# Kernel optimization log

Hardware: AMD Instinct MI355X
Metric: run time of the kernel (lower is better)

Reference implementation:

```python
import jax, jax.numpy as jnp
import numpy as np


def setup_inputs() -> dict:
    key = jax.random.key(0)
    k0, k1, k2, k3 = jax.random.split(key, 4)
    B, T, Din, H, Dout = 8, 4096, 1024, 1024, 1024
    x = jax.random.normal(k0, (B, T, Din), dtype=jnp.float32)
    # Linear weights stored torch-style as [out_features, in_features]
    W_hg = jax.random.normal(k1, (2 * H, Din), dtype=jnp.float32) * 0.02
    W_out = jax.random.normal(k2, (Dout, H), dtype=jnp.float32) * 0.02
    # episode-reset flags, 0/1 floats, shape [B,T,1] (expanded over channels)
    is_init = jax.random.bernoulli(k3, 0.01, (B, T, 1)).astype(jnp.float32)
    h_0 = jnp.zeros((B, 1, H), dtype=jnp.float32)
    return {"x": x, "W_hg": W_hg, "W_out": W_out, "is_init": is_init, "h_0": h_0}


def _mingru_scan(gate, hidden, is_init, h_0):
    # Linear recurrence h_t = (1-g_t) h_{t-1} + g_t * hidden_t, with resets.
    A = 1.0 - gate               # [B,T,H]
    Bv = gate * hidden           # [B,T,H]
    r = jnp.broadcast_to(is_init, Bv.shape)

    def combine(c1, c2):
        a1, b1, r1 = c1
        a2, b2, r2 = c2
        reset = r2 > 0
        a = jnp.where(reset, a2, a2 * a1)
        b = jnp.where(reset, b2, a2 * b1 + b2)
        return a, b, jnp.minimum(r1 + r2, 1.0)  # clamp(max=1)

    # Prepending the identity element then dropping it (as the torch code does)
    # is a no-op for an inclusive associative scan, so scan T elements directly.
    A_out, B_out, _ = jax.lax.associative_scan(combine, (A, Bv, r), axis=1)
    return A_out * h_0 + B_out   # h_0 is [B,1,H], broadcasts over T


def reference(x, W_hg, W_out, is_init, h_0):
    hg = jnp.einsum("btd,hd->bth", x, W_hg)          # [B,T,2H]
    hidden, gate = jnp.split(hg, 2, axis=-1)
    gate = jax.nn.sigmoid(gate)
    h = _mingru_scan(gate, hidden, is_init, h_0)      # [B,T,H]
    h_n = h[:, -1:]                                   # [B,1,H]
    out = jnp.einsum("bth,oh->bto", h, W_out)         # [B,T,Dout]
    return out, h_n
```

## Files before the change

kernel.cpp:

```cpp
#include <hip/hip_runtime.h>
#include <stdint.h>

#define B_DIM 8
#define T_DIM 4096
#define K_DIM 1024
#define H_DIM 1024
#define M_DIM (B_DIM * T_DIM)
#define CHUNK 64
#define NCHUNK (T_DIM / CHUNK)

typedef __attribute__((ext_vector_type(8))) short s16x8;
typedef __attribute__((ext_vector_type(4))) float f32x4;

__device__ __forceinline__ unsigned short f2b(float f) {
    union { float f; uint32_t u; } c; c.f = f;
    uint32_t r = (c.u + 0x7fffu + ((c.u >> 16) & 1u)) >> 16;
    return (unsigned short)r;
}
__device__ __forceinline__ float b2f(unsigned short u) {
    union { uint32_t u; float f; } c; c.u = ((uint32_t)u) << 16;
    return c.f;
}

__device__ __forceinline__ void gload_lds16(const unsigned short* g,
                                            unsigned short* l) {
    __builtin_amdgcn_global_load_lds(
        (__attribute__((address_space(1))) void*)g,
        (__attribute__((address_space(3))) void*)l, 16, 0, 0);
}

__device__ __forceinline__ void bar() {
    asm volatile("s_barrier" ::: "memory");
}


__global__ void cvt_f32_bf16(const float* __restrict__ src,
                             unsigned short* __restrict__ dst, int n4) {
    int stride = gridDim.x * blockDim.x;
    for (int i = blockIdx.x * blockDim.x + threadIdx.x; i < n4; i += stride) {
        float4 v = ((const float4*)src)[i];
        ushort4 o;
        o.x = f2b(v.x); o.y = f2b(v.y); o.z = f2b(v.z); o.w = f2b(v.w);
        ((ushort4*)dst)[i] = o;
    }
}

__global__ void prep_whg(const float* __restrict__ W,
                         unsigned short* __restrict__ Wp) {
    int i = blockIdx.x * blockDim.x + threadIdx.x;
    int total = 2 * H_DIM * K_DIM / 4;
    if (i >= total) return;
    int e = i * 4;
    int n = e >> 10;
    int k = e & 1023;
    int src = (n & 1) ? (H_DIM + (n >> 1)) : (n >> 1);
    float4 v = *(const float4*)&W[(size_t)src * K_DIM + k];
    ushort4 o;
    o.x = f2b(v.x); o.y = f2b(v.y); o.z = f2b(v.z); o.w = f2b(v.w);
    *(ushort4*)&Wp[(size_t)n * K_DIM + k] = o;
}


template <int EPI>
__global__ __launch_bounds__(512, 2) void gemm256(
    const unsigned short* __restrict__ A,
    const unsigned short* __restrict__ Bm,
    float* __restrict__ C,
    unsigned short* __restrict__ Sa,
    unsigned short* __restrict__ Sb,
    int N) {
    __shared__ unsigned short As[2][256 * 64];
    __shared__ unsigned short Bs[2][256 * 64];
    const int K = K_DIM;
    const int KT = K / 64;

    const int gx = gridDim.x;
    const int nwg = gx * gridDim.y;
    const int orig = blockIdx.y * gx + blockIdx.x;
    const int cpx = nwg >> 3;
    const int wg = (orig & 7) * cpx + (orig >> 3);
    const int m0 = (wg / gx) * 256;
    const int n0 = (wg % gx) * 256;

    const int t = threadIdx.x;
    const int lane = t & 63;
    const int w = t >> 6;
    const int wm = w >> 2, wn = w & 3;

    const int lrow = lane >> 3;
    const int lslot = (lane & 7) ^ lrow;

    const int l15 = lane & 15;
    const int rq = lane >> 4;
    const int rx = l15 & 7;

    f32x4 acc[8][4];
#pragma unroll
    for (int m = 0; m < 8; m++)
#pragma unroll
        for (int n = 0; n < 4; n++) acc[m][n] = (f32x4){0.f, 0.f, 0.f, 0.f};

    auto stageA = [&](int kt, int buf, int j) {
        const int seg = j * 8 + w;
        const int row = seg * 8 + lrow;
        gload_lds16(&A[(size_t)(m0 + row) * K + kt * 64 + lslot * 8],
                    &As[buf][seg * 512]);
    };
    auto stageB = [&](int kt, int buf, int j) {
        const int seg = j * 8 + w;
        const int row = seg * 8 + lrow;
        gload_lds16(&Bm[(size_t)(n0 + row) * K + kt * 64 + lslot * 8],
                    &Bs[buf][seg * 512]);
    };

    s16x8 af[4], bf[4];

#define LDA(buf, mi, ks) \
    (*(const s16x8*)&As[buf][(wm * 128 + (mi) * 16 + l15) * 64 + (((rq + (ks) * 4) ^ rx) * 8)])
#define LDB(buf, ni, ks) \
    (*(const s16x8*)&Bs[buf][(wn * 64 + (ni) * 16 + l15) * 64 + (((rq + (ks) * 4) ^ rx) * 8)])

#define MFMA16(MB)                                                          \
    __builtin_amdgcn_s_setprio(1);                                          \
    _Pragma("unroll") for (int m = 0; m < 4; m++)                           \
        _Pragma("unroll") for (int n = 0; n < 4; n++)                       \
            acc[MB + m][n] = __builtin_amdgcn_mfma_f32_16x16x32_bf16(       \
                af[m], bf[n], acc[MB + m][n], 0, 0, 0);                     \
    __builtin_amdgcn_s_setprio(0);

    {
#pragma unroll
        for (int j = 0; j < 4; j++) stageA(0, 0, j);
#pragma unroll
        for (int j = 0; j < 4; j++) stageB(0, 0, j);
        asm volatile("s_waitcnt vmcnt(0)" ::: "memory");
        bar();
    }

    for (int kt = 0; kt < KT; ++kt) {
        const int buf = kt & 1;
        const int nb = buf ^ 1;
        const bool nx = (kt + 1 < KT);
#pragma unroll
        for (int m = 0; m < 4; m++) af[m] = LDA(buf, m, 0);
#pragma unroll
        for (int n = 0; n < 4; n++) bf[n] = LDB(buf, n, 0);
        if (nx) { stageA(kt + 1, nb, 0); stageA(kt + 1, nb, 1); stageB(kt + 1, nb, 0); }
        bar();
        MFMA16(0);
        bar();
#pragma unroll
        for (int m = 0; m < 4; m++) af[m] = LDA(buf, m + 4, 0);
        if (nx) { stageA(kt + 1, nb, 2); stageA(kt + 1, nb, 3); stageB(kt + 1, nb, 1); }
        bar();
        MFMA16(4);
        bar();
#pragma unroll
        for (int m = 0; m < 4; m++) af[m] = LDA(buf, m, 1);
#pragma unroll
        for (int n = 0; n < 4; n++) bf[n] = LDB(buf, n, 1);
        if (nx) { stageB(kt + 1, nb, 2); stageB(kt + 1, nb, 3); }
        bar();
        MFMA16(0);
        bar();
#pragma unroll
        for (int m = 0; m < 4; m++) af[m] = LDA(buf, m + 4, 1);
        asm volatile("s_waitcnt vmcnt(0)" ::: "memory");
        bar();
        MFMA16(4);
        bar();
    }

    const int lr4 = rq * 4;
#pragma unroll
    for (int m = 0; m < 8; m++) {
#pragma unroll
        for (int n = 0; n < 4; n++) {
#pragma unroll
            for (int r = 0; r < 4; r++) {
                const int row = m0 + wm * 128 + m * 16 + lr4 + r;
                const int col = n0 + wn * 64 + n * 16 + l15;
                float v = acc[m][n][r];
                if (EPI == 0) {
                    C[(size_t)row * N + col] = v;
                } else {
                    float o = __shfl_xor(v, 1);
                    int ch = col >> 1;
                    if ((lane & 1) == 0) {
                        float g = 1.f / (1.f + __expf(-o));
                        Sb[(size_t)row * H_DIM + ch] = f2b(g * v);
                    } else {
                        float g = 1.f / (1.f + __expf(-v));
                        Sa[(size_t)row * H_DIM + ch] = f2b(1.f - g);
                    }
                }
            }
        }
    }
#undef LDA
#undef LDB
#undef MFMA16
}


__global__ __launch_bounds__(256) void scan_chunks(
    const unsigned short* __restrict__ Sa, const unsigned short* __restrict__ Sb,
    const float* __restrict__ is_init,
    float* __restrict__ CA, float* __restrict__ CB, float* __restrict__ CR) {
    int idx = blockIdx.x * 256 + threadIdx.x;
    int ch = idx & (H_DIM - 1);
    int chunk = (idx >> 10) & (NCHUNK - 1);
    int b = idx >> 16;
    int t0 = chunk * CHUNK;
    size_t base = ((size_t)b * T_DIM + t0) * H_DIM + ch;
    const float* ii = is_init + (size_t)b * T_DIM + t0;
    float A = 1.f, Bv = 0.f;
    int rf = 0;
    for (int i = 0; i < CHUNK; i++) {
        float a = b2f(Sa[base + (size_t)i * H_DIM]);
        float bb = b2f(Sb[base + (size_t)i * H_DIM]);
        bool rst = ii[i] > 0.f;
        A = rst ? a : a * A;
        Bv = rst ? bb : fmaf(a, Bv, bb);
        rf |= (int)rst;
    }
    size_t o = ((size_t)b * NCHUNK + chunk) * H_DIM + ch;
    CA[o] = A;
    CB[o] = Bv;
    if (ch == 0) CR[b * NCHUNK + chunk] = (float)rf;
}

__global__ void scan_tops(const float* __restrict__ CA, const float* __restrict__ CB,
                          const float* __restrict__ CR,
                          float* __restrict__ PA, float* __restrict__ PB) {
    int idx = blockIdx.x * blockDim.x + threadIdx.x;
    if (idx >= B_DIM * H_DIM) return;
    int ch = idx & (H_DIM - 1);
    int b = idx >> 10;
    float A = 1.f, Bv = 0.f;
    for (int c = 0; c < NCHUNK; c++) {
        size_t o = ((size_t)b * NCHUNK + c) * H_DIM + ch;
        PA[o] = A;
        PB[o] = Bv;
        float a = CA[o], bb = CB[o];
        bool rst = CR[b * NCHUNK + c] > 0.f;
        float nA = rst ? a : a * A;
        float nB = rst ? bb : fmaf(a, Bv, bb);
        A = nA; Bv = nB;
    }
}

__global__ __launch_bounds__(256) void scan_apply(
    const unsigned short* __restrict__ Sa, const unsigned short* __restrict__ Sb,
    const float* __restrict__ is_init,
    const float* __restrict__ PA, const float* __restrict__ PB,
    const float* __restrict__ h0,
    unsigned short* __restrict__ hb, float* __restrict__ hn) {
    int idx = blockIdx.x * 256 + threadIdx.x;
    int ch = idx & (H_DIM - 1);
    int chunk = (idx >> 10) & (NCHUNK - 1);
    int b = idx >> 16;
    int t0 = chunk * CHUNK;
    size_t base = ((size_t)b * T_DIM + t0) * H_DIM + ch;
    const float* ii = is_init + (size_t)b * T_DIM + t0;
    size_t po = ((size_t)b * NCHUNK + chunk) * H_DIM + ch;
    float A = PA[po], Bv = PB[po];
    float h0v = h0[b * H_DIM + ch];
    float h = 0.f;
    for (int i = 0; i < CHUNK; i++) {
        float a = b2f(Sa[base + (size_t)i * H_DIM]);
        float bb = b2f(Sb[base + (size_t)i * H_DIM]);
        bool rst = ii[i] > 0.f;
        A = rst ? a : a * A;
        Bv = rst ? bb : fmaf(a, Bv, bb);
        h = fmaf(A, h0v, Bv);
        hb[base + (size_t)i * H_DIM] = f2b(h);
    }
    if (chunk == NCHUNK - 1) hn[b * H_DIM + ch] = h;
}


extern "C" void kernel_launch(void* const* d_in, const int* in_sizes, int n_in,
                              void* d_out, int out_size, void* d_ws, size_t ws_size,
                              hipStream_t stream) {
    const float* x       = (const float*)d_in[0];
    const float* W_hg    = (const float*)d_in[1];
    const float* W_out   = (const float*)d_in[2];
    const float* is_init = (const float*)d_in[3];
    const float* h0      = (const float*)d_in[4];
    float* out = (float*)d_out;
    float* hn  = out + (size_t)M_DIM * H_DIM;

    char* ws = (char*)d_ws;
    size_t off = 0;
    auto alloc = [&](size_t bytes) {
        void* p = ws + off;
        off += (bytes + 255) & ~(size_t)255;
        return p;
    };
    unsigned short* xb  = (unsigned short*)alloc((size_t)M_DIM * K_DIM * 2);
    unsigned short* Wp  = (unsigned short*)alloc((size_t)2 * H_DIM * K_DIM * 2);
    unsigned short* Wob = (unsigned short*)alloc((size_t)H_DIM * K_DIM * 2);
    unsigned short* Sa  = (unsigned short*)alloc((size_t)M_DIM * H_DIM * 2);
    unsigned short* Sb  = (unsigned short*)alloc((size_t)M_DIM * H_DIM * 2);
    float* CA = (float*)alloc((size_t)B_DIM * NCHUNK * H_DIM * 4);
    float* CB = (float*)alloc((size_t)B_DIM * NCHUNK * H_DIM * 4);
    float* CR = (float*)alloc((size_t)B_DIM * NCHUNK * 4);
    float* PA = (float*)alloc((size_t)B_DIM * NCHUNK * H_DIM * 4);
    float* PB = (float*)alloc((size_t)B_DIM * NCHUNK * H_DIM * 4);
    unsigned short* hb = xb;

    cvt_f32_bf16<<<2048, 256, 0, stream>>>(x, xb, M_DIM * K_DIM / 4);
    prep_whg<<<(2 * H_DIM * K_DIM / 4 + 255) / 256, 256, 0, stream>>>(W_hg, Wp);
    cvt_f32_bf16<<<1024, 256, 0, stream>>>(W_out, Wob, H_DIM * K_DIM / 4);

    gemm256<1><<<dim3(2048 / 256, M_DIM / 256), 512, 0, stream>>>(
        xb, Wp, nullptr, Sa, Sb, 2048);

    scan_chunks<<<(B_DIM * NCHUNK * H_DIM) / 256, 256, 0, stream>>>(
        Sa, Sb, is_init, CA, CB, CR);
    scan_tops<<<(B_DIM * H_DIM + 255) / 256, 256, 0, stream>>>(CA, CB, CR, PA, PB);
    scan_apply<<<(B_DIM * NCHUNK * H_DIM) / 256, 256, 0, stream>>>(
        Sa, Sb, is_init, PA, PB, h0, hb, hn);

    gemm256<0><<<dim3(1024 / 256, M_DIM / 256), 512, 0, stream>>>(
        hb, Wob, out, nullptr, nullptr, 1024);
}
```

Measured before the change: 374.6 us.

## Restructure GEMM inner loop into two phases with both k-slices loaded

The k-tile loop in the bf16 MFMA GEMM now has two phases instead of four. Each phase loads both k-substeps of A and B fragments from LDS into separate register sets, then issues 32 MFMAs per barrier pair. Global-to-LDS staging is regrouped so all of A is prefetched in the first phase and all of B in the second, with explicit lgkmcnt waits and sched_barriers. The aim is fewer workgroup barriers and longer MFMA runs, at the cost of extra VGPRs for the doubled fragment registers, which could lower occupancy.

```diff
diff --git a/kernel.cpp b/kernel.cpp
--- a/kernel.cpp
+++ b/kernel.cpp
@@ -113,19 +113,23 @@
                     &Bs[buf][seg * 512]);
     };
 
-    s16x8 af[4], bf[4];
+    s16x8 af0[4], af1[4], bf0[4], bf1[4];
 
 #define LDA(buf, mi, ks) \
     (*(const s16x8*)&As[buf][(wm * 128 + (mi) * 16 + l15) * 64 + (((rq + (ks) * 4) ^ rx) * 8)])
 #define LDB(buf, ni, ks) \
     (*(const s16x8*)&Bs[buf][(wn * 64 + (ni) * 16 + l15) * 64 + (((rq + (ks) * 4) ^ rx) * 8)])
 
-#define MFMA16(MB)                                                          \
+#define MFMA32(MB)                                                          \
     __builtin_amdgcn_s_setprio(1);                                          \
     _Pragma("unroll") for (int m = 0; m < 4; m++)                           \
         _Pragma("unroll") for (int n = 0; n < 4; n++)                       \
             acc[MB + m][n] = __builtin_amdgcn_mfma_f32_16x16x32_bf16(       \
-                af[m], bf[n], acc[MB + m][n], 0, 0, 0);                     \
+                af0[m], bf0[n], acc[MB + m][n], 0, 0, 0);                   \
+    _Pragma("unroll") for (int m = 0; m < 4; m++)                           \
+        _Pragma("unroll") for (int n = 0; n < 4; n++)                       \
+            acc[MB + m][n] = __builtin_amdgcn_mfma_f32_16x16x32_bf16(       \
+                af1[m], bf1[n], acc[MB + m][n], 0, 0, 0);                   \
     __builtin_amdgcn_s_setprio(0);
 
     {
@@ -142,32 +146,31 @@
         const int nb = buf ^ 1;
         const bool nx = (kt + 1 < KT);
 #pragma unroll
-        for (int m = 0; m < 4; m++) af[m] = LDA(buf, m, 0);
-#pragma unroll
-        for (int n = 0; n < 4; n++) bf[n] = LDB(buf, n, 0);
-        if (nx) { stageA(kt + 1, nb, 0); stageA(kt + 1, nb, 1); stageB(kt + 1, nb, 0); }
-        bar();
-        MFMA16(0);
-        bar();
-#pragma unroll
-        for (int m = 0; m < 4; m++) af[m] = LDA(buf, m + 4, 0);
-        if (nx) { stageA(kt + 1, nb, 2); stageA(kt + 1, nb, 3); stageB(kt + 1, nb, 1); }
-        bar();
-        MFMA16(4);
-        bar();
-#pragma unroll
-        for (int m = 0; m < 4; m++) af[m] = LDA(buf, m, 1);
-#pragma unroll
-        for (int n = 0; n < 4; n++) bf[n] = LDB(buf, n, 1);
-        if (nx) { stageB(kt + 1, nb, 2); stageB(kt + 1, nb, 3); }
-        bar();
-        MFMA16(0);
-        bar();
-#pragma unroll
-        for (int m = 0; m < 4; m++) af[m] = LDA(buf, m + 4, 1);
+        for (int m = 0; m < 4; m++) { af0[m] = LDA(buf, m, 0); af1[m] = LDA(buf, m, 1); }
+#pragma unroll
+        for (int n = 0; n < 4; n++) { bf0[n] = LDB(buf, n, 0); bf1[n] = LDB(buf, n, 1); }
+        if (nx) {
+#pragma unroll
+            for (int j = 0; j < 4; j++) stageA(kt + 1, nb, j);
+        }
+        asm volatile("s_waitcnt lgkmcnt(8)" ::: "memory");
+        bar();
+        asm volatile("s_waitcnt lgkmcnt(0)" ::: "memory");
+        __builtin_amdgcn_sched_barrier(0);
+        MFMA32(0);
+        bar();
+#pragma unroll
+        for (int m = 0; m < 4; m++) { af0[m] = LDA(buf, m + 4, 0); af1[m] = LDA(buf, m + 4, 1); }
+        if (nx) {
+#pragma unroll
+            for (int j = 0; j < 4; j++) stageB(kt + 1, nb, j);
+        }
+        asm volatile("s_waitcnt lgkmcnt(4)" ::: "memory");
+        bar();
+        asm volatile("s_waitcnt lgkmcnt(0)" ::: "memory");
+        __builtin_amdgcn_sched_barrier(0);
+        MFMA32(4);
         asm volatile("s_waitcnt vmcnt(0)" ::: "memory");
-        bar();
-        MFMA16(4);
         bar();
     }
 
@@ -199,7 +202,7 @@
     }
 #undef LDA
 #undef LDB
-#undef MFMA16
+#undef MFMA32
 }
 
 
```

After: 396.2 us. 1.06x slower.

## Restage GEMM LDS into four half-K slots with deeper vmcnt-gated prefetch

Applied to the files above, without the earlier changes.

Splits each 64-wide K tile into two 32-wide halves held in a 4-slot LDS ring, using a lane-contiguous layout per 16-row block instead of the XOR-swizzled 64-wide layout. Global-to-LDS loads are issued further ahead and throttled with partial vmcnt waits rather than a full drain each iteration. Explicit lgkmcnt waits and sched barriers fence each MFMA phase. The aim is to hide more global-load latency. The risks are LDS bank conflicts from dropping the swizzle and extra synchronisation overhead.

```diff
diff --git a/kernel.cpp b/kernel.cpp
--- a/kernel.cpp
+++ b/kernel.cpp
@@ -69,8 +69,8 @@
     unsigned short* __restrict__ Sa,
     unsigned short* __restrict__ Sb,
     int N) {
-    __shared__ unsigned short As[2][256 * 64];
-    __shared__ unsigned short Bs[2][256 * 64];
+    __shared__ unsigned short As4[4][256 * 32];
+    __shared__ unsigned short Bs4[4][256 * 32];
     const int K = K_DIM;
     const int KT = K / 64;
 
@@ -87,12 +87,11 @@
     const int w = t >> 6;
     const int wm = w >> 2, wn = w & 3;
 
-    const int lrow = lane >> 3;
-    const int lslot = (lane & 7) ^ lrow;
+    const int srow = lane & 15;
+    const int sq   = lane >> 4;
 
     const int l15 = lane & 15;
     const int rq = lane >> 4;
-    const int rx = l15 & 7;
 
     f32x4 acc[8][4];
 #pragma unroll
@@ -100,76 +99,75 @@
 #pragma unroll
         for (int n = 0; n < 4; n++) acc[m][n] = (f32x4){0.f, 0.f, 0.f, 0.f};
 
-    auto stageA = [&](int kt, int buf, int j) {
-        const int seg = j * 8 + w;
-        const int row = seg * 8 + lrow;
-        gload_lds16(&A[(size_t)(m0 + row) * K + kt * 64 + lslot * 8],
-                    &As[buf][seg * 512]);
+    auto stageA = [&](int kt, int ks, int j) {
+        const int slot = (2 * kt + ks) & 3;
+        const int row = j * 128 + w * 16 + srow;
+        const int gk  = kt * 64 + ks * 32 + sq * 8;
+        gload_lds16(&A[(size_t)(m0 + row) * K + gk],
+                    &As4[slot][(j * 128 + w * 16) * 32]);
     };
-    auto stageB = [&](int kt, int buf, int j) {
-        const int seg = j * 8 + w;
-        const int row = seg * 8 + lrow;
-        gload_lds16(&Bm[(size_t)(n0 + row) * K + kt * 64 + lslot * 8],
-                    &Bs[buf][seg * 512]);
+    auto stageB = [&](int kt, int ks, int j) {
+        const int slot = (2 * kt + ks) & 3;
+        const int row = j * 128 + w * 16 + srow;
+        const int gk  = kt * 64 + ks * 32 + sq * 8;
+        gload_lds16(&Bm[(size_t)(n0 + row) * K + gk],
+                    &Bs4[slot][(j * 128 + w * 16) * 32]);
     };
 
     s16x8 af[4], bf[4];
 
-#define LDA(buf, mi, ks) \
-    (*(const s16x8*)&As[buf][(wm * 128 + (mi) * 16 + l15) * 64 + (((rq + (ks) * 4) ^ rx) * 8)])
-#define LDB(buf, ni, ks) \
-    (*(const s16x8*)&Bs[buf][(wn * 64 + (ni) * 16 + l15) * 64 + (((rq + (ks) * 4) ^ rx) * 8)])
-
-#define MFMA16(MB)                                                          \
+#define LDAX(S, MI) \
+    (*(const s16x8*)&As4[S][(wm * 8 + (MI)) * 512 + rq * 128 + l15 * 8])
+#define LDBX(S, NI) \
+    (*(const s16x8*)&Bs4[S][(wn * 4 + (NI)) * 512 + rq * 128 + l15 * 8])
+
+#define LGKM0 do { asm volatile("s_waitcnt lgkmcnt(0)" ::: "memory"); \
+                   __builtin_amdgcn_sched_barrier(0); } while (0)
+#define VMW8 asm volatile("s_waitcnt vmcnt(8)" ::: "memory")
+#define VMW4 asm volatile("s_waitcnt vmcnt(4)" ::: "memory")
+#define VMW0 asm volatile("s_waitcnt vmcnt(0)" ::: "memory")
+
+#define PH_MFMA(MB) do {                                                    \
     __builtin_amdgcn_s_setprio(1);                                          \
-    _Pragma("unroll") for (int m = 0; m < 4; m++)                           \
-        _Pragma("unroll") for (int n = 0; n < 4; n++)                       \
-            acc[MB + m][n] = __builtin_amdgcn_mfma_f32_16x16x32_bf16(       \
-                af[m], bf[n], acc[MB + m][n], 0, 0, 0);                     \
-    __builtin_amdgcn_s_setprio(0);
-
-    {
-#pragma unroll
-        for (int j = 0; j < 4; j++) stageA(0, 0, j);
-#pragma unroll
-        for (int j = 0; j < 4; j++) stageB(0, 0, j);
-        asm volatile("s_waitcnt vmcnt(0)" ::: "memory");
-        bar();
-    }
-
-    for (int kt = 0; kt < KT; ++kt) {
-        const int buf = kt & 1;
-        const int nb = buf ^ 1;
-        const bool nx = (kt + 1 < KT);
-#pragma unroll
-        for (int m = 0; m < 4; m++) af[m] = LDA(buf, m, 0);
-#pragma unroll
-        for (int n = 0; n < 4; n++) bf[n] = LDB(buf, n, 0);
-        if (nx) { stageA(kt + 1, nb, 0); stageA(kt + 1, nb, 1); stageB(kt + 1, nb, 0); }
-        bar();
-        MFMA16(0);
-        bar();
-#pragma unroll
-        for (int m = 0; m < 4; m++) af[m] = LDA(buf, m + 4, 0);
-        if (nx) { stageA(kt + 1, nb, 2); stageA(kt + 1, nb, 3); stageB(kt + 1, nb, 1); }
-        bar();
-        MFMA16(4);
-        bar();
-#pragma unroll
-        for (int m = 0; m < 4; m++) af[m] = LDA(buf, m, 1);
-#pragma unroll
-        for (int n = 0; n < 4; n++) bf[n] = LDB(buf, n, 1);
-        if (nx) { stageB(kt + 1, nb, 2); stageB(kt + 1, nb, 3); }
-        bar();
-        MFMA16(0);
-        bar();
-#pragma unroll
-        for (int m = 0; m < 4; m++) af[m] = LDA(buf, m + 4, 1);
-        asm volatile("s_waitcnt vmcnt(0)" ::: "memory");
-        bar();
-        MFMA16(4);
-        bar();
-    }
+    _Pragma("unroll") for (int m_ = 0; m_ < 4; m_++)                        \
+        _Pragma("unroll") for (int n_ = 0; n_ < 4; n_++)                    \
+            acc[(MB) + m_][n_] = __builtin_amdgcn_mfma_f32_16x16x32_bf16(   \
+                af[m_], bf[n_], acc[(MB) + m_][n_], 0, 0, 0);               \
+    __builtin_amdgcn_s_setprio(0);                                          \
+} while (0)
+
+#define ISSUE_U(KT_, KS_) do {                                              \
+    stageA((KT_), (KS_), 0); stageA((KT_), (KS_), 1);                       \
+    stageB((KT_), (KS_), 0); stageB((KT_), (KS_), 1);                       \
+} while (0)
+
+#define TILE(KT_, ISS1, ISS3, VM2, VM4) do {                                \
+    const int s0_ = (2 * (KT_)) & 3, s1_ = (2 * (KT_) + 1) & 3;             \
+    _Pragma("unroll") for (int m_ = 0; m_ < 4; m_++) af[m_] = LDAX(s0_, m_);\
+    _Pragma("unroll") for (int n_ = 0; n_ < 4; n_++) bf[n_] = LDBX(s0_, n_);\
+    ISS1;                                                                   \
+    bar(); LGKM0; PH_MFMA(0); bar();                                        \
+    _Pragma("unroll") for (int m_ = 0; m_ < 4; m_++) af[m_] = LDAX(s0_, m_ + 4); \
+    bar(); LGKM0; PH_MFMA(4); VM2; bar();                                   \
+    _Pragma("unroll") for (int m_ = 0; m_ < 4; m_++) af[m_] = LDAX(s1_, m_);\
+    _Pragma("unroll") for (int n_ = 0; n_ < 4; n_++) bf[n_] = LDBX(s1_, n_);\
+    ISS3;                                                                   \
+    bar(); LGKM0; PH_MFMA(0); bar();                                        \
+    _Pragma("unroll") for (int m_ = 0; m_ < 4; m_++) af[m_] = LDAX(s1_, m_ + 4); \
+    bar(); LGKM0; PH_MFMA(4); VM4; bar();                                   \
+} while (0)
+
+    ISSUE_U(0, 0);
+    ISSUE_U(0, 1);
+    ISSUE_U(1, 0);
+    VMW8;
+    bar();
+
+    for (int kt = 0; kt < KT - 2; ++kt) {
+        TILE(kt, ISSUE_U(kt + 1, 1), ISSUE_U(kt + 2, 0), VMW8, VMW8);
+    }
+    TILE(KT - 2, ISSUE_U(KT - 1, 1), ((void)0), VMW8, VMW4);
+    TILE(KT - 1, ((void)0), ((void)0), VMW0, ((void)0));
 
     const int lr4 = rq * 4;
 #pragma unroll
@@ -197,9 +195,11 @@
             }
         }
     }
-#undef LDA
-#undef LDB
-#undef MFMA16
+#undef LDAX
+#undef LDBX
+#undef TILE
+#undef PH_MFMA
+#undef ISSUE_U
 }
 
 
```

New measurement: 474.6 us. +26.7%, slower.

## Fuse three-pass chunked scan into single-pass decoupled look-back kernel

Applied to the files above, without the earlier changes.

Replaces the chunk-reduce, top-level scan and apply kernels with one kernel that claims chunks through an atomic ticket. Each chunk keeps its 64 gate/value pairs in registers, publishes its aggregate or inclusive end state, and walks back over predecessor status flags. The GEMM epilogue now writes a packed bf16 (a,b) pair per element, so the scan reads a single 32-bit word instead of two separate arrays. The aim is to read Sa/Sb once instead of twice and to drop the serial per-batch tops kernel and two launches. In exchange it adds spin-waiting on flags, a 64-register array per thread, and a dependence on forward-progress ordering via the ticket counter.

```diff
diff --git a/kernel.cpp b/kernel.cpp
--- a/kernel.cpp
+++ b/kernel.cpp
@@ -60,14 +60,18 @@
     *(ushort4*)&Wp[(size_t)n * K_DIM + k] = o;
 }
 
+__global__ void zero_flags(int* f, int n) {
+    int i = blockIdx.x * blockDim.x + threadIdx.x;
+    if (i < n) f[i] = 0;
+}
+
 
 template <int EPI>
 __global__ __launch_bounds__(512, 2) void gemm256(
     const unsigned short* __restrict__ A,
     const unsigned short* __restrict__ Bm,
     float* __restrict__ C,
-    unsigned short* __restrict__ Sa,
-    unsigned short* __restrict__ Sb,
+    uint32_t* __restrict__ Sab,
     int N) {
     __shared__ unsigned short As[2][256 * 64];
     __shared__ unsigned short Bs[2][256 * 64];
@@ -185,13 +189,11 @@
                     C[(size_t)row * N + col] = v;
                 } else {
                     float o = __shfl_xor(v, 1);
-                    int ch = col >> 1;
                     if ((lane & 1) == 0) {
                         float g = 1.f / (1.f + __expf(-o));
-                        Sb[(size_t)row * H_DIM + ch] = f2b(g * v);
-                    } else {
-                        float g = 1.f / (1.f + __expf(-v));
-                        Sa[(size_t)row * H_DIM + ch] = f2b(1.f - g);
+                        uint32_t pk = (uint32_t)f2b(1.f - g) |
+                                      ((uint32_t)f2b(g * v) << 16);
+                        Sab[(size_t)row * H_DIM + (col >> 1)] = pk;
                     }
                 }
             }
@@ -203,80 +205,111 @@
 }
 
 
-__global__ __launch_bounds__(256) void scan_chunks(
-    const unsigned short* __restrict__ Sa, const unsigned short* __restrict__ Sb,
-    const float* __restrict__ is_init,
-    float* __restrict__ CA, float* __restrict__ CB, float* __restrict__ CR) {
-    int idx = blockIdx.x * 256 + threadIdx.x;
-    int ch = idx & (H_DIM - 1);
-    int chunk = (idx >> 10) & (NCHUNK - 1);
-    int b = idx >> 16;
-    int t0 = chunk * CHUNK;
-    size_t base = ((size_t)b * T_DIM + t0) * H_DIM + ch;
+__global__ __launch_bounds__(1024) void scan_fused(
+    const uint32_t* __restrict__ Sab, const float* __restrict__ is_init,
+    const float* __restrict__ h0,
+    uint32_t* __restrict__ aggA, uint32_t* __restrict__ aggB,
+    uint32_t* __restrict__ hend, int* __restrict__ status,
+    int* __restrict__ ticket,
+    unsigned short* __restrict__ hb, float* __restrict__ hn) {
+    __shared__ int s_tick;
+    __shared__ int s_st;
+    if (threadIdx.x == 0) s_tick = atomicAdd(ticket, 1);
+    __syncthreads();
+    const int bc = s_tick;
+    const int b = bc >> 6;
+    const int c = bc & 63;
+    const int ch = threadIdx.x;
+    const int t0 = c * CHUNK;
+    const size_t base = ((size_t)b * T_DIM + t0) * H_DIM + ch;
     const float* ii = is_init + (size_t)b * T_DIM + t0;
+    const float h0v = h0[b * H_DIM + ch];
+
+    uint32_t d[CHUNK];
+#pragma unroll
+    for (int i = 0; i < CHUNK; i++) d[i] = Sab[base + (size_t)i * H_DIM];
+
     float A = 1.f, Bv = 0.f;
     int rf = 0;
+#pragma unroll
     for (int i = 0; i < CHUNK; i++) {
-        float a = b2f(Sa[base + (size_t)i * H_DIM]);
-        float bb = b2f(Sb[base + (size_t)i * H_DIM]);
+        float a = b2f((unsigned short)(d[i] & 0xffffu));
+        float bb = b2f((unsigned short)(d[i] >> 16));
         bool rst = ii[i] > 0.f;
         A = rst ? a : a * A;
         Bv = rst ? bb : fmaf(a, Bv, bb);
         rf |= (int)rst;
     }
-    size_t o = ((size_t)b * NCHUNK + chunk) * H_DIM + ch;
-    CA[o] = A;
-    CB[o] = Bv;
-    if (ch == 0) CR[b * NCHUNK + chunk] = (float)rf;
-}
-
-__global__ void scan_tops(const float* __restrict__ CA, const float* __restrict__ CB,
-                          const float* __restrict__ CR,
-                          float* __restrict__ PA, float* __restrict__ PB) {
-    int idx = blockIdx.x * blockDim.x + threadIdx.x;
-    if (idx >= B_DIM * H_DIM) return;
-    int ch = idx & (H_DIM - 1);
-    int b = idx >> 10;
-    float A = 1.f, Bv = 0.f;
-    for (int c = 0; c < NCHUNK; c++) {
-        size_t o = ((size_t)b * NCHUNK + c) * H_DIM + ch;
-        PA[o] = A;
-        PB[o] = Bv;
-        float a = CA[o], bb = CB[o];
-        bool rst = CR[b * NCHUNK + c] > 0.f;
-        float nA = rst ? a : a * A;
-        float nB = rst ? bb : fmaf(a, Bv, bb);
-        A = nA; Bv = nB;
-    }
-}
-
-__global__ __launch_bounds__(256) void scan_apply(
-    const unsigned short* __restrict__ Sa, const unsigned short* __restrict__ Sb,
-    const float* __restrict__ is_init,
-    const float* __restrict__ PA, const float* __restrict__ PB,
-    const float* __restrict__ h0,
-    unsigned short* __restrict__ hb, float* __restrict__ hn) {
-    int idx = blockIdx.x * 256 + threadIdx.x;
-    int ch = idx & (H_DIM - 1);
-    int chunk = (idx >> 10) & (NCHUNK - 1);
-    int b = idx >> 16;
-    int t0 = chunk * CHUNK;
-    size_t base = ((size_t)b * T_DIM + t0) * H_DIM + ch;
-    const float* ii = is_init + (size_t)b * T_DIM + t0;
-    size_t po = ((size_t)b * NCHUNK + chunk) * H_DIM + ch;
-    float A = PA[po], Bv = PB[po];
-    float h0v = h0[b * H_DIM + ch];
-    float h = 0.f;
+
+    const bool inc_now = (c == 0) || rf;
+    if (inc_now) {
+        __hip_atomic_store(&hend[(size_t)bc * H_DIM + ch],
+                           __float_as_uint(fmaf(A, h0v, Bv)),
+                           __ATOMIC_RELAXED, __HIP_MEMORY_SCOPE_AGENT);
+    } else {
+        __hip_atomic_store(&aggA[(size_t)bc * H_DIM + ch], __float_as_uint(A),
+                           __ATOMIC_RELAXED, __HIP_MEMORY_SCOPE_AGENT);
+        __hip_atomic_store(&aggB[(size_t)bc * H_DIM + ch], __float_as_uint(Bv),
+                           __ATOMIC_RELAXED, __HIP_MEMORY_SCOPE_AGENT);
+    }
+    __syncthreads();
+    if (threadIdx.x == 0)
+        __hip_atomic_store(&status[bc], inc_now ? 2 : 1,
+                           __ATOMIC_RELEASE, __HIP_MEMORY_SCOPE_AGENT);
+
+    float hentry = h0v;
+    if (c > 0) {
+        float sA = 1.f, sB = 0.f;
+        int p = bc - 1;
+        for (;;) {
+            if (threadIdx.x == 0) {
+                int st;
+                while ((st = __hip_atomic_load(&status[p], __ATOMIC_ACQUIRE,
+                                               __HIP_MEMORY_SCOPE_AGENT)) == 0)
+                    __builtin_amdgcn_s_sleep(4);
+                s_st = st;
+            }
+            __syncthreads();
+            int st = s_st;
+            __syncthreads();
+            if (st == 2) {
+                float he = __uint_as_float(__hip_atomic_load(
+                    &hend[(size_t)p * H_DIM + ch], __ATOMIC_RELAXED,
+                    __HIP_MEMORY_SCOPE_AGENT));
+                hentry = fmaf(sA, he, sB);
+                break;
+            }
+            float ea = __uint_as_float(__hip_atomic_load(
+                &aggA[(size_t)p * H_DIM + ch], __ATOMIC_RELAXED,
+                __HIP_MEMORY_SCOPE_AGENT));
+            float eb = __uint_as_float(__hip_atomic_load(
+                &aggB[(size_t)p * H_DIM + ch], __ATOMIC_RELAXED,
+                __HIP_MEMORY_SCOPE_AGENT));
+            sB = fmaf(sA, eb, sB);
+            sA = sA * ea;
+            p--;
+        }
+    }
+
+    float h = hentry;
+#pragma unroll
     for (int i = 0; i < CHUNK; i++) {
-        float a = b2f(Sa[base + (size_t)i * H_DIM]);
-        float bb = b2f(Sb[base + (size_t)i * H_DIM]);
+        float a = b2f((unsigned short)(d[i] & 0xffffu));
+        float bb = b2f((unsigned short)(d[i] >> 16));
         bool rst = ii[i] > 0.f;
-        A = rst ? a : a * A;
-        Bv = rst ? bb : fmaf(a, Bv, bb);
-        h = fmaf(A, h0v, Bv);
+        h = fmaf(a, rst ? h0v : h, bb);
         hb[base + (size_t)i * H_DIM] = f2b(h);
     }
-    if (chunk == NCHUNK - 1) hn[b * H_DIM + ch] = h;
+
+    if (!inc_now) {
+        __hip_atomic_store(&hend[(size_t)bc * H_DIM + ch], __float_as_uint(h),
+                           __ATOMIC_RELAXED, __HIP_MEMORY_SCOPE_AGENT);
+        __syncthreads();
+        if (threadIdx.x == 0)
+            __hip_atomic_store(&status[bc], 2,
+                               __ATOMIC_RELEASE, __HIP_MEMORY_SCOPE_AGENT);
+    }
+    if (c == NCHUNK - 1) hn[b * H_DIM + ch] = h;
 }
 
 
@@ -301,28 +334,28 @@
     unsigned short* xb  = (unsigned short*)alloc((size_t)M_DIM * K_DIM * 2);
     unsigned short* Wp  = (unsigned short*)alloc((size_t)2 * H_DIM * K_DIM * 2);
     unsigned short* Wob = (unsigned short*)alloc((size_t)H_DIM * K_DIM * 2);
-    unsigned short* Sa  = (unsigned short*)alloc((size_t)M_DIM * H_DIM * 2);
-    unsigned short* Sb  = (unsigned short*)alloc((size_t)M_DIM * H_DIM * 2);
-    float* CA = (float*)alloc((size_t)B_DIM * NCHUNK * H_DIM * 4);
-    float* CB = (float*)alloc((size_t)B_DIM * NCHUNK * H_DIM * 4);
-    float* CR = (float*)alloc((size_t)B_DIM * NCHUNK * 4);
-    float* PA = (float*)alloc((size_t)B_DIM * NCHUNK * H_DIM * 4);
-    float* PB = (float*)alloc((size_t)B_DIM * NCHUNK * H_DIM * 4);
+    uint32_t* Sab = (uint32_t*)alloc((size_t)M_DIM * H_DIM * 4);
+    uint32_t* aggA = (uint32_t*)alloc((size_t)B_DIM * NCHUNK * H_DIM * 4);
+    uint32_t* aggB = (uint32_t*)alloc((size_t)B_DIM * NCHUNK * H_DIM * 4);
+    uint32_t* hend = (uint32_t*)alloc((size_t)B_DIM * NCHUNK * H_DIM * 4);
+    int* flags = (int*)alloc(1024 * 4);
     unsigned short* hb = xb;
+
+    int* status = flags;
+    int* ticket = flags + 512;
+
+    zero_flags<<<1, 1024, 0, stream>>>(flags, 1024);
 
     cvt_f32_bf16<<<2048, 256, 0, stream>>>(x, xb, M_DIM * K_DIM / 4);
     prep_whg<<<(2 * H_DIM * K_DIM / 4 + 255) / 256, 256, 0, stream>>>(W_hg, Wp);
     cvt_f32_bf16<<<1024, 256, 0, stream>>>(W_out, Wob, H_DIM * K_DIM / 4);
 
     gemm256<1><<<dim3(2048 / 256, M_DIM / 256), 512, 0, stream>>>(
-        xb, Wp, nullptr, Sa, Sb, 2048);
-
-    scan_chunks<<<(B_DIM * NCHUNK * H_DIM) / 256, 256, 0, stream>>>(
-        Sa, Sb, is_init, CA, CB, CR);
-    scan_tops<<<(B_DIM * H_DIM + 255) / 256, 256, 0, stream>>>(CA, CB, CR, PA, PB);
-    scan_apply<<<(B_DIM * NCHUNK * H_DIM) / 256, 256, 0, stream>>>(
-        Sa, Sb, is_init, PA, PB, h0, hb, hn);
+        xb, Wp, nullptr, Sab, 2048);
+
+    scan_fused<<<B_DIM * NCHUNK, 1024, 0, stream>>>(
+        Sab, is_init, h0, aggA, aggB, hend, status, ticket, hb, hn);
 
     gemm256<0><<<dim3(1024 / 256, M_DIM / 256), 512, 0, stream>>>(
-        hb, Wob, out, nullptr, nullptr, 1024);
-}
+        hb, Wob, out, nullptr, 1024);
+}
```

After: 394.4 us. +5.3%, slower.
